# Optimization experiments

Measured on AMD Instinct MI355X. Metric: run time of the kernel, lower is better.

Reference implementation:

```python
import jax, jax.numpy as jnp
import numpy as np

N_NODES = 50000
N_EDGES = 800000


def gat_layer(h, src, dst, W, al, ar, b, n_dst):
    # h: [N, Fin]; W: [Fin, H*D]; al/ar: [H, D]; b: [H*D]
    H, D = al.shape
    z = (h @ W).reshape(-1, H, D)                      # [N, H, D]
    el = jnp.sum(z * al[None], axis=-1)                # [N, H]
    er = jnp.sum(z * ar[None], axis=-1)                # [N, H] (dst prefix == all nodes)
    e = jax.nn.leaky_relu(el[src] + er[dst], negative_slope=0.2)  # [E, H]
    emax = jax.ops.segment_max(e, dst, num_segments=n_dst)
    ee = jnp.exp(e - emax[dst])
    denom = jax.ops.segment_sum(ee, dst, num_segments=n_dst)
    alpha = ee / denom[dst]                            # [E, H]
    msg = alpha[:, :, None] * z[src]                   # [E, H, D]
    out = jax.ops.segment_sum(msg.reshape(-1, H * D), dst, num_segments=n_dst)
    return out + b                                     # [n_dst, H*D]


def setup_inputs() -> dict:
    key = jax.random.key(0)
    ks = jax.random.split(key, 16)
    hid, heads, dh = 256, 4, 64
    inp = {
        "x": jax.random.normal(ks[0], (N_NODES, 128), jnp.float32),
        "conv0_W": jax.random.normal(ks[1], (128, hid), jnp.float32) * 0.08,
        "conv0_al": jax.random.normal(ks[2], (heads, dh), jnp.float32) * 0.1,
        "conv0_ar": jax.random.normal(ks[3], (heads, dh), jnp.float32) * 0.1,
        "conv0_b": jnp.zeros((hid,), jnp.float32),
        "skip0_W": jax.random.normal(ks[4], (128, hid), jnp.float32) * 0.08,
        "skip0_b": jnp.zeros((hid,), jnp.float32),
        "conv1_W": jax.random.normal(ks[5], (hid, hid), jnp.float32) * 0.06,
        "conv1_al": jax.random.normal(ks[6], (heads, dh), jnp.float32) * 0.1,
        "conv1_ar": jax.random.normal(ks[7], (heads, dh), jnp.float32) * 0.1,
        "conv1_b": jnp.zeros((hid,), jnp.float32),
        "skip1_W": jax.random.normal(ks[8], (hid, hid), jnp.float32) * 0.06,
        "skip1_b": jnp.zeros((hid,), jnp.float32),
        "mlp_W1": jax.random.normal(ks[9], (hid, hid), jnp.float32) * 0.06,
        "mlp_b1": jnp.zeros((hid,), jnp.float32),
        "bn_gamma": jnp.ones((hid,), jnp.float32),
        "bn_beta": jnp.zeros((hid,), jnp.float32),
        "bn_mean": jnp.zeros((hid,), jnp.float32),
        "bn_var": jnp.ones((hid,), jnp.float32),
        "mlp_W2": jax.random.normal(ks[10], (hid, 47), jnp.float32) * 0.06,
        "mlp_b2": jnp.zeros((47,), jnp.float32),
        "edge_src": jax.random.randint(ks[11], (N_EDGES,), 0, N_NODES, jnp.int32),
        "edge_dst": jax.random.randint(ks[12], (N_EDGES,), 0, N_NODES, jnp.int32),
    }
    return inp


def reference(x, conv0_W, conv0_al, conv0_ar, conv0_b, skip0_W, skip0_b,
              conv1_W, conv1_al, conv1_ar, conv1_b, skip1_W, skip1_b,
              mlp_W1, mlp_b1, bn_gamma, bn_beta, bn_mean, bn_var,
              mlp_W2, mlp_b2, edge_src, edge_dst):
    n = x.shape[0]
    # layer 0: GAT conv + skip + ELU (dropout = identity in eval mode)
    h = gat_layer(x, edge_src, edge_dst, conv0_W, conv0_al, conv0_ar, conv0_b, n)
    h = jax.nn.elu(h + x @ skip0_W + skip0_b)
    # layer 1
    g = gat_layer(h, edge_src, edge_dst, conv1_W, conv1_al, conv1_ar, conv1_b, n)
    h = jax.nn.elu(g + h @ skip1_W + skip1_b)
    # MLP head: Linear -> BN(eval) -> ReLU -> (dropout id) -> Linear
    m = h @ mlp_W1 + mlp_b1
    m = (m - bn_mean) * (bn_gamma / jnp.sqrt(bn_var + 1e-5)) + bn_beta
    m = jax.nn.relu(m)
    logits = m @ mlp_W2 + mlp_b2
    return jax.nn.log_softmax(logits, axis=-1)
```

## Files before the change

### kernel.cpp

```cpp
#include <hip/hip_runtime.h>
#include <math.h>

#define NN 50000
#define NE 800000
#define HID 256
#define NH 4
#define DH 64
#define NB 196
#define CHUNK 4082

static inline int cdiv(int a, int b) { return (a + b - 1) / b; }

typedef __attribute__((ext_vector_type(8))) short short8;
typedef __attribute__((ext_vector_type(4))) short short4v;
typedef __attribute__((ext_vector_type(4))) float f32x4;
typedef __attribute__((ext_vector_type(2))) float f32x2;

__device__ inline unsigned short f2bf(float x) {
    union { float f; unsigned u; } v; v.f = x;
    unsigned r = v.u + 0x7FFFu + ((v.u >> 16) & 1u);
    return (unsigned short)(r >> 16);
}
__device__ inline float bf2f(unsigned short h) {
    union { unsigned u; float f; } v; v.u = ((unsigned)h) << 16;
    return v.f;
}
__device__ inline short8 zero8() {
    short8 z;
#pragma unroll
    for (int j = 0; j < 8; j++) z[j] = 0;
    return z;
}
__device__ inline unsigned char f2fp8(float x) {
    int p = __builtin_amdgcn_cvt_pk_fp8_f32(x, 0.f, 0, false);
    return (unsigned char)(p & 0xff);
}

__global__ __launch_bounds__(256) void p1_bucket_hist(const int* __restrict__ dst,
                                                      int* __restrict__ bcount) {
    __shared__ int h[NB];
    int tid = threadIdx.x;
    for (int i = tid; i < NB; i += 256) h[i] = 0;
    __syncthreads();
    int i0 = blockIdx.x * CHUNK;
    int n = min(CHUNK, NE - i0);
    for (int i = tid; i < n; i += 256) atomicAdd(&h[dst[i0 + i] >> 8], 1);
    __syncthreads();
    for (int i = tid; i < NB; i += 256)
        if (h[i]) atomicAdd(&bcount[i], h[i]);
}

__global__ __launch_bounds__(256) void p2_bucket_scan(const int* __restrict__ bcount,
                                                      int* __restrict__ bbase,
                                                      int* __restrict__ gcur) {
    __shared__ int s[256];
    int tid = threadIdx.x;
    int v = (tid < NB) ? bcount[tid] : 0;
    s[tid] = v;
    __syncthreads();
    for (int off = 1; off < 256; off <<= 1) {
        int t = (tid >= off) ? s[tid - off] : 0;
        __syncthreads();
        s[tid] += t;
        __syncthreads();
    }
    int ex = s[tid] - v;
    if (tid < NB) { bbase[tid] = ex; gcur[tid] = ex; }
    if (tid == NB - 1) bbase[NB] = s[tid];
}

__global__ __launch_bounds__(256) void p3_partition(
    const int* __restrict__ src, const int* __restrict__ dst,
    int* __restrict__ gcur, uint2* __restrict__ ebuf) {
    __shared__ int cnt[NB], loff[NB], cur[NB], gpos[NB];
    __shared__ int s[256];
    __shared__ uint2 buf[CHUNK];
    int tid = threadIdx.x;
    int i0 = blockIdx.x * CHUNK;
    int n = min(CHUNK, NE - i0);
    for (int i = tid; i < NB; i += 256) cnt[i] = 0;
    __syncthreads();
    for (int i = tid; i < n; i += 256) atomicAdd(&cnt[dst[i0 + i] >> 8], 1);
    __syncthreads();
    int v = (tid < NB) ? cnt[tid] : 0;
    s[tid] = v;
    __syncthreads();
    for (int off = 1; off < 256; off <<= 1) {
        int t = (tid >= off) ? s[tid - off] : 0;
        __syncthreads();
        s[tid] += t;
        __syncthreads();
    }
    if (tid < NB) {
        int ex = s[tid] - v;
        loff[tid] = ex;
        cur[tid] = ex;
        gpos[tid] = v ? atomicAdd(&gcur[tid], v) : 0;
    }
    __syncthreads();
    for (int i = tid; i < n; i += 256) {
        int d = dst[i0 + i];
        int sv = src[i0 + i];
        int p = atomicAdd(&cur[d >> 8], 1);
        buf[p] = make_uint2((unsigned)sv, (unsigned)d);
    }
    __syncthreads();
    for (int i = tid; i < n; i += 256) {
        uint2 e = buf[i];
        int b = (int)(e.y >> 8);
        ebuf[gpos[b] + (i - loff[b])] = e;
    }
}

__global__ __launch_bounds__(256) void p4_bucket_csr(
    const uint2* __restrict__ ebuf, const int* __restrict__ bbase,
    int* __restrict__ row_ptr, int* __restrict__ csr_src) {
    __shared__ int hist[256], cur[256], s[256];
    int b = blockIdx.x;
    int tid = threadIdx.x;
    int e0 = bbase[b], e1 = bbase[b + 1];
    hist[tid] = 0;
    __syncthreads();
    for (int i = e0 + tid; i < e1; i += 256)
        atomicAdd(&hist[ebuf[i].y & 255], 1);
    __syncthreads();
    int v = hist[tid];
    s[tid] = v;
    __syncthreads();
    for (int off = 1; off < 256; off <<= 1) {
        int t = (tid >= off) ? s[tid - off] : 0;
        __syncthreads();
        s[tid] += t;
        __syncthreads();
    }
    int pre = s[tid] - v;
    cur[tid] = pre;
    int d = b * 256 + tid;
    if (d < NN) row_ptr[d] = e0 + pre;
    if (b == NB - 1 && tid == 0) row_ptr[NN] = NE;
    __syncthreads();
    for (int i = e0 + tid; i < e1; i += 256) {
        uint2 e = ebuf[i];
        int p = atomicAdd(&cur[e.y & 255], 1);
        csr_src[e0 + p] = (int)e.x;
    }
}

__global__ void wcast_all_kernel(
    const float* __restrict__ c0W, const float* __restrict__ s0W,
    const float* __restrict__ c1W, const float* __restrict__ s1W,
    const float* __restrict__ m1W, const float* __restrict__ W2,
    const float* __restrict__ x,
    unsigned short* __restrict__ c0h, unsigned short* __restrict__ s0h,
    unsigned short* __restrict__ c1h, unsigned short* __restrict__ s1h,
    unsigned short* __restrict__ m1h, unsigned short* __restrict__ hWh,
    unsigned short* __restrict__ xh) {
    int i = blockIdx.x * blockDim.x + threadIdx.x;
    if (i >= 278528) {
        int j = i - 278528;
        if (j >= NN * 128 / 4) return;
        float4 v = ((const float4*)x)[j];
        short4v h;
        h[0] = (short)f2bf(v.x); h[1] = (short)f2bf(v.y);
        h[2] = (short)f2bf(v.z); h[3] = (short)f2bf(v.w);
        *(short4v*)&xh[j * 4] = h;
        return;
    }
    const float* W; unsigned short* H; int base; int head = 0;
    if (i < 32768)        { W = c0W; H = c0h; base = i; }
    else if (i < 65536)   { W = s0W; H = s0h; base = i - 32768; }
    else if (i < 131072)  { W = c1W; H = c1h; base = i - 65536; }
    else if (i < 196608)  { W = s1W; H = s1h; base = i - 131072; }
    else if (i < 262144)  { W = m1W; H = m1h; base = i - 196608; }
    else                  { W = W2;  H = hWh; base = i - 262144; head = 1; }
    float x_; int off;
    if (!head) {
        int k = base >> 8, n = base & 255;
        x_ = W[base];
        off = (k >> 5) * 8192 + (n >> 4) * 512 + ((k >> 3) & 3) * 128 + (n & 15) * 8 + (k & 7);
    } else {
        int k = base >> 6, n = base & 63;
        x_ = (n < 47) ? W[k * 47 + n] : 0.f;
        off = (k >> 5) * 2048 + (n >> 4) * 512 + ((k >> 3) & 3) * 128 + (n & 15) * 8 + (k & 7);
    }
    H[off] = f2bf(x_);
}

__global__ __launch_bounds__(256) void gemm_fused_kernel(
    const unsigned short* __restrict__ Ah,
    const unsigned short* __restrict__ Wc, const unsigned short* __restrict__ Ws,
    int M, int K,
    unsigned char* __restrict__ zb, unsigned short* __restrict__ sraw,
    const float* __restrict__ al, const float* __restrict__ ar,
    float* __restrict__ el, float* __restrict__ er) {
    __shared__ short sA[2][1024];

    int tid = threadIdx.x;
    int lane = tid & 63;
    int wid = tid >> 6;
    int m0 = blockIdx.x * 32;

    f32x4 accc[2][4], accs[2][4];
#pragma unroll
    for (int i = 0; i < 2; i++)
#pragma unroll
        for (int j = 0; j < 4; j++) {
            accc[i][j] = (f32x4){0.f, 0.f, 0.f, 0.f};
            accs[i][j] = (f32x4){0.f, 0.f, 0.f, 0.f};
        }

    bool stager = (tid < 128);
    int t7 = tid & 127;
    int r = t7 >> 2, kq = t7 & 3;
    int gr = m0 + r;
    size_t abase = (size_t)gr * K + kq * 8;
    int aoff = (r >> 4) * 512 + kq * 128 + (r & 15) * 8;

    int nkt = K >> 5;
    if (stager) {
        short8 sreg = zero8();
        if (gr < M) sreg = *(const short8*)(Ah + abase);
        *(short8*)(&sA[0][0] + aoff) = sreg;
    }
    __syncthreads();

    const unsigned short* bcp = Wc + (wid * 4) * 512 + lane * 8;
    const unsigned short* bsp = Ws + (wid * 4) * 512 + lane * 8;

    for (int kt = 0; kt < nkt; kt++) {
        short8 nreg = zero8();
        if (stager && kt + 1 < nkt && gr < M)
            nreg = *(const short8*)(Ah + abase + (size_t)(kt + 1) * 32);
        short8 bc[4], bs[4];
#pragma unroll
        for (int nf = 0; nf < 4; nf++) {
            bc[nf] = *(const short8*)(bcp + kt * 8192 + nf * 512);
            bs[nf] = *(const short8*)(bsp + kt * 8192 + nf * 512);
        }
        const short* cur = &sA[kt & 1][0];
        short8 ah[2];
#pragma unroll
        for (int mf = 0; mf < 2; mf++)
            ah[mf] = *(const short8*)(cur + mf * 512 + lane * 8);
#pragma unroll
        for (int nf = 0; nf < 4; nf++)
#pragma unroll
            for (int mf = 0; mf < 2; mf++) {
                accc[mf][nf] = __builtin_amdgcn_mfma_f32_16x16x32_bf16(ah[mf], bc[nf], accc[mf][nf], 0, 0, 0);
                accs[mf][nf] = __builtin_amdgcn_mfma_f32_16x16x32_bf16(ah[mf], bs[nf], accs[mf][nf], 0, 0, 0);
            }
        if (stager && kt + 1 < nkt)
            *(short8*)(&sA[(kt + 1) & 1][0] + aoff) = nreg;
        __syncthreads();
    }

#pragma unroll
    for (int mf = 0; mf < 2; mf++) {
        int row0 = m0 + mf * 16 + (lane >> 4) * 4;
#pragma unroll
        for (int reg = 0; reg < 4; reg++) {
            int row = row0 + reg;
            if (row >= M) continue;
            size_t rb = (size_t)row * HID;
#pragma unroll
            for (int nf = 0; nf < 4; nf++) {
                int col = wid * 64 + nf * 16 + (lane & 15);
                zb[rb + col] = f2fp8(accc[mf][nf][reg]);
                sraw[rb + col] = f2bf(accs[mf][nf][reg]);
            }
        }
    }

    {
        float alv[4], arv[4];
#pragma unroll
        for (int nf = 0; nf < 4; nf++) {
            int col = wid * 64 + nf * 16 + (lane & 15);
            alv[nf] = al[col];
            arv[nf] = ar[col];
        }
#pragma unroll
        for (int mf = 0; mf < 2; mf++) {
#pragma unroll
            for (int reg = 0; reg < 4; reg++) {
                float pl = 0.f, pr = 0.f;
#pragma unroll
                for (int nf = 0; nf < 4; nf++) {
                    pl = fmaf(accc[mf][nf][reg], alv[nf], pl);
                    pr = fmaf(accc[mf][nf][reg], arv[nf], pr);
                }
#pragma unroll
                for (int off = 8; off; off >>= 1) {
                    pl += __shfl_xor(pl, off);
                    pr += __shfl_xor(pr, off);
                }
                int row = m0 + mf * 16 + (lane >> 4) * 4 + reg;
                if ((lane & 15) == 0 && row < M) {
                    el[row * 4 + wid] = pl;
                    er[row * 4 + wid] = pr;
                }
            }
        }
    }
}

__global__ __launch_bounds__(256) void aggregate_kernel(
    const int* __restrict__ row_ptr, const int* __restrict__ csr_src,
    const float4* __restrict__ el4, const float4* __restrict__ er4,
    const unsigned char* __restrict__ zb, const float* __restrict__ conv_b,
    const unsigned short* __restrict__ sraw, const float* __restrict__ skip_b,
    unsigned short* __restrict__ outh, int n) {
    __shared__ float s_w[4][NH][64];
    __shared__ int s_s[4][64];
    int wid = threadIdx.x >> 6;
    int lane = threadIdx.x & 63;
    int node = blockIdx.x * 4 + wid;
    if (node >= n) return;
    int rb = row_ptr[node];
    int deg = row_ptr[node + 1] - rb;
    float4 ern = er4[node];
    float er_h[NH] = {ern.x, ern.y, ern.z, ern.w};
    int myh = lane >> 4;
    int f0 = lane * 4;

    float4 acc = make_float4(0.f, 0.f, 0.f, 0.f);
    float wsum[NH] = {0.f, 0.f, 0.f, 0.f};

    for (int c = 0; c < deg; c += 64) {
        int i = c + lane;
        int cnt = min(64, deg - c);
        if (i < deg) {
            int s = csr_src[rb + i];
            s_s[wid][lane] = s;
            float4 elv = el4[s];
            float ev[NH] = {elv.x, elv.y, elv.z, elv.w};
#pragma unroll
            for (int h = 0; h < NH; h++) {
                float e = ev[h] + er_h[h];
                e = (e > 0.f) ? e : 0.2f * e;
                float ee = __expf(e);
                s_w[wid][h][lane] = ee;
                wsum[h] += ee;
            }
        }
        __builtin_amdgcn_wave_barrier();
#pragma unroll 2
        for (int e = 0; e < cnt; e++) {
            int s = s_s[wid][e];
            unsigned zu = *(const unsigned*)(zb + (size_t)s * HID + f0);
            float wgt = s_w[wid][myh][e];
            f32x2 lo = __builtin_amdgcn_cvt_pk_f32_fp8((int)zu, false);
            f32x2 hi = __builtin_amdgcn_cvt_pk_f32_fp8((int)zu, true);
            acc.x = fmaf(wgt, lo[0], acc.x);
            acc.y = fmaf(wgt, lo[1], acc.y);
            acc.z = fmaf(wgt, hi[0], acc.z);
            acc.w = fmaf(wgt, hi[1], acc.w);
        }
        __builtin_amdgcn_wave_barrier();
    }
#pragma unroll
    for (int h = 0; h < NH; h++)
#pragma unroll
        for (int off = 32; off; off >>= 1) wsum[h] += __shfl_xor(wsum[h], off);
    float inv = (wsum[myh] > 0.f) ? 1.f / wsum[myh] : 0.f;
    float4 cb = *(const float4*)(conv_b + f0);
    float4 sb = *(const float4*)(skip_b + f0);
    uint2 sv = *(const uint2*)(sraw + (size_t)node * HID + f0);
    union { unsigned u; float f; } s0, s1, s2, s3;
    s0.u = sv.x << 16; s1.u = sv.x & 0xffff0000u;
    s2.u = sv.y << 16; s3.u = sv.y & 0xffff0000u;
    float v0 = acc.x * inv + cb.x + s0.f + sb.x;
    float v1 = acc.y * inv + cb.y + s1.f + sb.y;
    float v2 = acc.z * inv + cb.z + s2.f + sb.z;
    float v3 = acc.w * inv + cb.w + s3.f + sb.w;
    v0 = (v0 > 0.f) ? v0 : expm1f(v0);
    v1 = (v1 > 0.f) ? v1 : expm1f(v1);
    v2 = (v2 > 0.f) ? v2 : expm1f(v2);
    v3 = (v3 > 0.f) ? v3 : expm1f(v3);
    short4v o;
    o[0] = (short)f2bf(v0); o[1] = (short)f2bf(v1);
    o[2] = (short)f2bf(v2); o[3] = (short)f2bf(v3);
    *(short4v*)(outh + (size_t)node * HID + f0) = o;
}

__global__ __launch_bounds__(256) void gemm_bn_kernel(
    const unsigned short* __restrict__ Ah, const unsigned short* __restrict__ Bh_g,
    int M, int K, unsigned short* __restrict__ C,
    const float* __restrict__ bias, const float* __restrict__ g,
    const float* __restrict__ bt, const float* __restrict__ mean,
    const float* __restrict__ var) {
    __shared__ short sA[2][1024];
    int tid = threadIdx.x;
    int lane = tid & 63;
    int wid = tid >> 6;
    int m0 = blockIdx.x * 32;

    f32x4 acc[2][4];
#pragma unroll
    for (int i = 0; i < 2; i++)
#pragma unroll
        for (int j = 0; j < 4; j++) acc[i][j] = (f32x4){0.f, 0.f, 0.f, 0.f};

    bool stager = (tid < 128);
    int t7 = tid & 127;
    int r = t7 >> 2, kq = t7 & 3;
    int gr = m0 + r;
    size_t abase = (size_t)gr * K + kq * 8;
    int aoff = (r >> 4) * 512 + kq * 128 + (r & 15) * 8;

    int nkt = K >> 5;
    if (stager) {
        short8 sreg = zero8();
        if (gr < M) sreg = *(const short8*)(Ah + abase);
        *(short8*)(&sA[0][0] + aoff) = sreg;
    }
    __syncthreads();

    const unsigned short* bhp = Bh_g + (wid * 4) * 512 + lane * 8;

    for (int kt = 0; kt < nkt; kt++) {
        short8 nreg = zero8();
        if (stager && kt + 1 < nkt && gr < M)
            nreg = *(const short8*)(Ah + abase + (size_t)(kt + 1) * 32);
        short8 bh[4];
#pragma unroll
        for (int nf = 0; nf < 4; nf++)
            bh[nf] = *(const short8*)(bhp + kt * 8192 + nf * 512);
        const short* cur = &sA[kt & 1][0];
        short8 ah[2];
#pragma unroll
        for (int mf = 0; mf < 2; mf++)
            ah[mf] = *(const short8*)(cur + mf * 512 + lane * 8);
#pragma unroll
        for (int nf = 0; nf < 4; nf++)
#pragma unroll
            for (int mf = 0; mf < 2; mf++)
                acc[mf][nf] = __builtin_amdgcn_mfma_f32_16x16x32_bf16(ah[mf], bh[nf], acc[mf][nf], 0, 0, 0);
        if (stager && kt + 1 < nkt)
            *(short8*)(&sA[(kt + 1) & 1][0] + aoff) = nreg;
        __syncthreads();
    }

#pragma unroll
    for (int mf = 0; mf < 2; mf++) {
        int row0 = m0 + mf * 16 + (lane >> 4) * 4;
#pragma unroll
        for (int reg = 0; reg < 4; reg++) {
            int row = row0 + reg;
            if (row >= M) continue;
            size_t rb = (size_t)row * HID;
#pragma unroll
            for (int nf = 0; nf < 4; nf++) {
                int col = wid * 64 + nf * 16 + (lane & 15);
                float v = acc[mf][nf][reg];
                float s = g[col] * rsqrtf(var[col] + 1e-5f);
                v = (v + bias[col] - mean[col]) * s + bt[col];
                C[rb + col] = f2bf(fmaxf(v, 0.f));
            }
        }
    }
}

__global__ __launch_bounds__(256) void head_kernel(
    const unsigned short* __restrict__ Ah, const unsigned short* __restrict__ Bh_g,
    const float* __restrict__ b2, float* __restrict__ out, int M) {
    __shared__ short sA[2048];
    int tid = threadIdx.x;
    int lane = tid & 63;
    int wid = tid >> 6;
    int m0 = blockIdx.x * 64;

    f32x4 acc[4];
#pragma unroll
    for (int nf = 0; nf < 4; nf++) acc[nf] = (f32x4){0.f, 0.f, 0.f, 0.f};

    for (int kt = 0; kt < 8; kt++) {
        {
            int r = tid >> 2, kq = tid & 3;
            int gr = m0 + r;
            short8 h8 = zero8();
            if (gr < M) h8 = *(const short8*)(Ah + (size_t)gr * HID + kt * 32 + kq * 8);
            int off = (r >> 4) * 512 + kq * 128 + (r & 15) * 8;
            *(short8*)&sA[off] = h8;
        }
        __syncthreads();
        short8 ah = *(const short8*)&sA[wid * 512 + lane * 8];
#pragma unroll
        for (int nf = 0; nf < 4; nf++) {
            short8 bh = *(const short8*)(Bh_g + kt * 2048 + nf * 512 + lane * 8);
            acc[nf] = __builtin_amdgcn_mfma_f32_16x16x32_bf16(ah, bh, acc[nf], 0, 0, 0);
        }
        __syncthreads();
    }

    int col0 = lane & 15;
    float bias_[4];
#pragma unroll
    for (int nf = 0; nf < 4; nf++) {
        int col = nf * 16 + col0;
        bias_[nf] = (col < 47) ? b2[col] : 0.f;
    }
#pragma unroll
    for (int reg = 0; reg < 4; reg++) {
        int row = m0 + wid * 16 + (lane >> 4) * 4 + reg;
        float lg[4];
        float mx = -INFINITY;
#pragma unroll
        for (int nf = 0; nf < 4; nf++) {
            int col = nf * 16 + col0;
            float v = acc[nf][reg] + bias_[nf];
            lg[nf] = v;
            if (col < 47) mx = fmaxf(mx, v);
        }
#pragma unroll
        for (int off = 8; off; off >>= 1) mx = fmaxf(mx, __shfl_xor(mx, off));
        float s = 0.f;
#pragma unroll
        for (int nf = 0; nf < 4; nf++) {
            int col = nf * 16 + col0;
            if (col < 47) s += __expf(lg[nf] - mx);
        }
#pragma unroll
        for (int off = 8; off; off >>= 1) s += __shfl_xor(s, off);
        float li = logf(s);
        if (row < M) {
#pragma unroll
            for (int nf = 0; nf < 3; nf++) {
                int col = nf * 16 + col0;
                if (col < 47) out[(size_t)row * 47 + col] = lg[nf] - mx - li;
            }
        }
    }
}

extern "C" void kernel_launch(void* const* d_in, const int* in_sizes, int n_in,
                              void* d_out, int out_size, void* d_ws, size_t ws_size,
                              hipStream_t stream) {
    const float* x        = (const float*)d_in[0];
    const float* conv0_W  = (const float*)d_in[1];
    const float* conv0_al = (const float*)d_in[2];
    const float* conv0_ar = (const float*)d_in[3];
    const float* conv0_b  = (const float*)d_in[4];
    const float* skip0_W  = (const float*)d_in[5];
    const float* skip0_b  = (const float*)d_in[6];
    const float* conv1_W  = (const float*)d_in[7];
    const float* conv1_al = (const float*)d_in[8];
    const float* conv1_ar = (const float*)d_in[9];
    const float* conv1_b  = (const float*)d_in[10];
    const float* skip1_W  = (const float*)d_in[11];
    const float* skip1_b  = (const float*)d_in[12];
    const float* mlp_W1   = (const float*)d_in[13];
    const float* mlp_b1   = (const float*)d_in[14];
    const float* bn_gamma = (const float*)d_in[15];
    const float* bn_beta  = (const float*)d_in[16];
    const float* bn_mean  = (const float*)d_in[17];
    const float* bn_var   = (const float*)d_in[18];
    const float* mlp_W2   = (const float*)d_in[19];
    const float* mlp_b2   = (const float*)d_in[20];
    const int* edge_src   = (const int*)d_in[21];
    const int* edge_dst   = (const int*)d_in[22];
    float* out = (float*)d_out;

    char* w = (char*)d_ws;
    size_t off = 0;
    auto alloc = [&](size_t bytes) {
        char* p = w + off;
        off += (bytes + 255) & ~(size_t)255;
        return p;
    };
    int*    row_ptr = (int*)alloc((NN + 1) * sizeof(int));
    int*    bcount  = (int*)alloc(256 * sizeof(int));
    int*    bbase   = (int*)alloc(256 * sizeof(int));
    int*    gcur    = (int*)alloc(256 * sizeof(int));
    int*    csr_src = (int*)alloc(NE * sizeof(int));
    uint2*  ebuf    = (uint2*)alloc((size_t)NE * sizeof(uint2));
    float*  el      = (float*)alloc((size_t)NN * 4 * sizeof(float));
    float*  er      = (float*)alloc((size_t)NN * 4 * sizeof(float));
    unsigned char*  zb   = (unsigned char*)alloc((size_t)NN * HID * 2);
    unsigned short* sraw = (unsigned short*)alloc((size_t)NN * HID * 2);
    unsigned short* slA  = (unsigned short*)alloc((size_t)NN * HID * 2);
    unsigned short* hh   = (unsigned short*)alloc((size_t)NN * HID * 2);
    unsigned short* c0h = (unsigned short*)alloc(128 * 256 * 2);
    unsigned short* s0h = (unsigned short*)alloc(128 * 256 * 2);
    unsigned short* c1h = (unsigned short*)alloc(256 * 256 * 2);
    unsigned short* s1h = (unsigned short*)alloc(256 * 256 * 2);
    unsigned short* m1h = (unsigned short*)alloc(256 * 256 * 2);
    unsigned short* hWh = (unsigned short*)alloc(256 * 64 * 2);
    (void)ws_size;

    unsigned short* xh  = slA;
    unsigned short* h2h = slA;
    unsigned short* mh  = (unsigned short*)zb;

    int gemm_grid = cdiv(NN, 32);
    int head_grid = cdiv(NN, 64);
    int nodeblocks = cdiv(NN, 4);

    wcast_all_kernel<<<cdiv(278528 + NN * 128 / 4, 256), 256, 0, stream>>>(
        conv0_W, skip0_W, conv1_W, skip1_W, mlp_W1, mlp_W2, x,
        c0h, s0h, c1h, s1h, m1h, hWh, xh);

    hipMemsetAsync(bcount, 0, 256 * sizeof(int), stream);
    p1_bucket_hist<<<NB, 256, 0, stream>>>(edge_dst, bcount);
    p2_bucket_scan<<<1, 256, 0, stream>>>(bcount, bbase, gcur);
    p3_partition<<<NB, 256, 0, stream>>>(edge_src, edge_dst, gcur, ebuf);
    p4_bucket_csr<<<NB, 256, 0, stream>>>(ebuf, bbase, row_ptr, csr_src);

    gemm_fused_kernel<<<gemm_grid, 256, 0, stream>>>(xh, c0h, s0h, NN, 128,
        zb, sraw, conv0_al, conv0_ar, el, er);
    aggregate_kernel<<<nodeblocks, 256, 0, stream>>>(row_ptr, csr_src,
        (const float4*)el, (const float4*)er, zb, conv0_b, sraw, skip0_b, hh, NN);

    gemm_fused_kernel<<<gemm_grid, 256, 0, stream>>>(hh, c1h, s1h, NN, 256,
        zb, sraw, conv1_al, conv1_ar, el, er);
    aggregate_kernel<<<nodeblocks, 256, 0, stream>>>(row_ptr, csr_src,
        (const float4*)el, (const float4*)er, zb, conv1_b, sraw, skip1_b, h2h, NN);

    gemm_bn_kernel<<<gemm_grid, 256, 0, stream>>>(h2h, m1h, NN, 256,
        mh, mlp_b1, bn_gamma, bn_beta, bn_mean, bn_var);
    head_kernel<<<head_grid, 256, 0, stream>>>(mh, hWh, mlp_b2, out, NN);
}
```

Before: 246.4 us.

## Process four edges per wave in aggregation with 16-byte fp8 row loads

Restructures the GAT aggregation so each wave splits into four 16-lane groups, each handling a different neighbor edge, with every lane loading 16 fp8 features as a uint4 instead of 4 bytes. Edge scores are computed one head per lane group in 16-edge chunks, and partial accumulators are combined across groups with cross-lane shuffles at the end. The aim is more memory-level parallelism and wider gather loads for the feature rows. The cost is 16 accumulator registers per lane, a cross-group reduction, and select logic to pick outputs.

```diff
diff --git a/kernel.cpp b/kernel.cpp
--- a/kernel.cpp
+++ b/kernel.cpp
@@ -306,73 +306,102 @@
 
 __global__ __launch_bounds__(256) void aggregate_kernel(
     const int* __restrict__ row_ptr, const int* __restrict__ csr_src,
-    const float4* __restrict__ el4, const float4* __restrict__ er4,
+    const float* __restrict__ el, const float4* __restrict__ er4,
     const unsigned char* __restrict__ zb, const float* __restrict__ conv_b,
     const unsigned short* __restrict__ sraw, const float* __restrict__ skip_b,
     unsigned short* __restrict__ outh, int n) {
-    __shared__ float s_w[4][NH][64];
-    __shared__ int s_s[4][64];
+    __shared__ float s_w[4][NH][16];
+    __shared__ int s_s[4][16];
     int wid = threadIdx.x >> 6;
     int lane = threadIdx.x & 63;
     int node = blockIdx.x * 4 + wid;
     if (node >= n) return;
     int rb = row_ptr[node];
     int deg = row_ptr[node + 1] - rb;
+    int sl = lane & 15;
+    int grp = lane >> 4;
+    int myh = sl >> 2;
     float4 ern = er4[node];
-    float er_h[NH] = {ern.x, ern.y, ern.z, ern.w};
-    int myh = lane >> 4;
-    int f0 = lane * 4;
-
-    float4 acc = make_float4(0.f, 0.f, 0.f, 0.f);
-    float wsum[NH] = {0.f, 0.f, 0.f, 0.f};
-
-    for (int c = 0; c < deg; c += 64) {
-        int i = c + lane;
-        int cnt = min(64, deg - c);
+    float erh = (grp == 0) ? ern.x : (grp == 1) ? ern.y : (grp == 2) ? ern.z : ern.w;
+
+    float acc[16];
+#pragma unroll
+    for (int j = 0; j < 16; j++) acc[j] = 0.f;
+    float wloc = 0.f;
+
+    for (int c = 0; c < deg; c += 16) {
+        int i = c + sl;
+        int cnt = min(16, deg - c);
         if (i < deg) {
             int s = csr_src[rb + i];
-            s_s[wid][lane] = s;
-            float4 elv = el4[s];
-            float ev[NH] = {elv.x, elv.y, elv.z, elv.w};
-#pragma unroll
-            for (int h = 0; h < NH; h++) {
-                float e = ev[h] + er_h[h];
-                e = (e > 0.f) ? e : 0.2f * e;
-                float ee = __expf(e);
-                s_w[wid][h][lane] = ee;
-                wsum[h] += ee;
+            if (grp == 0) s_s[wid][sl] = s;
+            float e = el[(s << 2) + grp] + erh;
+            e = (e > 0.f) ? e : 0.2f * e;
+            float ee = __expf(e);
+            s_w[wid][grp][sl] = ee;
+            wloc += ee;
+        }
+        __builtin_amdgcn_wave_barrier();
+        for (int e4 = 0; e4 < cnt; e4 += 4) {
+            int ei = e4 + grp;
+            if (ei < cnt) {
+                int s = s_s[wid][ei];
+                float wgt = s_w[wid][myh][ei];
+                uint4 zv = *(const uint4*)(zb + (size_t)s * HID + sl * 16);
+                f32x2 d0 = __builtin_amdgcn_cvt_pk_f32_fp8((int)zv.x, false);
+                f32x2 d1 = __builtin_amdgcn_cvt_pk_f32_fp8((int)zv.x, true);
+                f32x2 d2 = __builtin_amdgcn_cvt_pk_f32_fp8((int)zv.y, false);
+                f32x2 d3 = __builtin_amdgcn_cvt_pk_f32_fp8((int)zv.y, true);
+                f32x2 d4 = __builtin_amdgcn_cvt_pk_f32_fp8((int)zv.z, false);
+                f32x2 d5 = __builtin_amdgcn_cvt_pk_f32_fp8((int)zv.z, true);
+                f32x2 d6 = __builtin_amdgcn_cvt_pk_f32_fp8((int)zv.w, false);
+                f32x2 d7 = __builtin_amdgcn_cvt_pk_f32_fp8((int)zv.w, true);
+                acc[0]  = fmaf(wgt, d0[0], acc[0]);
+                acc[1]  = fmaf(wgt, d0[1], acc[1]);
+                acc[2]  = fmaf(wgt, d1[0], acc[2]);
+                acc[3]  = fmaf(wgt, d1[1], acc[3]);
+                acc[4]  = fmaf(wgt, d2[0], acc[4]);
+                acc[5]  = fmaf(wgt, d2[1], acc[5]);
+                acc[6]  = fmaf(wgt, d3[0], acc[6]);
+                acc[7]  = fmaf(wgt, d3[1], acc[7]);
+                acc[8]  = fmaf(wgt, d4[0], acc[8]);
+                acc[9]  = fmaf(wgt, d4[1], acc[9]);
+                acc[10] = fmaf(wgt, d5[0], acc[10]);
+                acc[11] = fmaf(wgt, d5[1], acc[11]);
+                acc[12] = fmaf(wgt, d6[0], acc[12]);
+                acc[13] = fmaf(wgt, d6[1], acc[13]);
+                acc[14] = fmaf(wgt, d7[0], acc[14]);
+                acc[15] = fmaf(wgt, d7[1], acc[15]);
             }
         }
         __builtin_amdgcn_wave_barrier();
-#pragma unroll 2
-        for (int e = 0; e < cnt; e++) {
-            int s = s_s[wid][e];
-            unsigned zu = *(const unsigned*)(zb + (size_t)s * HID + f0);
-            float wgt = s_w[wid][myh][e];
-            f32x2 lo = __builtin_amdgcn_cvt_pk_f32_fp8((int)zu, false);
-            f32x2 hi = __builtin_amdgcn_cvt_pk_f32_fp8((int)zu, true);
-            acc.x = fmaf(wgt, lo[0], acc.x);
-            acc.y = fmaf(wgt, lo[1], acc.y);
-            acc.z = fmaf(wgt, hi[0], acc.z);
-            acc.w = fmaf(wgt, hi[1], acc.w);
-        }
-        __builtin_amdgcn_wave_barrier();
-    }
-#pragma unroll
-    for (int h = 0; h < NH; h++)
-#pragma unroll
-        for (int off = 32; off; off >>= 1) wsum[h] += __shfl_xor(wsum[h], off);
-    float inv = (wsum[myh] > 0.f) ? 1.f / wsum[myh] : 0.f;
-    float4 cb = *(const float4*)(conv_b + f0);
-    float4 sb = *(const float4*)(skip_b + f0);
-    uint2 sv = *(const uint2*)(sraw + (size_t)node * HID + f0);
+    }
+
+#pragma unroll
+    for (int off = 1; off < 16; off <<= 1) wloc += __shfl_xor(wloc, off);
+    float wsum_my = __shfl(wloc, myh << 4);
+    float inv = (wsum_my > 0.f) ? 1.f / wsum_my : 0.f;
+
+#pragma unroll
+    for (int j = 0; j < 16; j++) {
+        acc[j] += __shfl_xor(acc[j], 16);
+        acc[j] += __shfl_xor(acc[j], 32);
+    }
+
+#define SELA(k) ((grp & 2) ? ((grp & 1) ? acc[12 + (k)] : acc[8 + (k)]) \
+                           : ((grp & 1) ? acc[4 + (k)]  : acc[0 + (k)]))
+    int g0 = (sl << 4) + (grp << 2);
+    float4 cb = *(const float4*)(conv_b + g0);
+    float4 sb = *(const float4*)(skip_b + g0);
+    uint2 sv = *(const uint2*)(sraw + (size_t)node * HID + g0);
     union { unsigned u; float f; } s0, s1, s2, s3;
     s0.u = sv.x << 16; s1.u = sv.x & 0xffff0000u;
     s2.u = sv.y << 16; s3.u = sv.y & 0xffff0000u;
-    float v0 = acc.x * inv + cb.x + s0.f + sb.x;
-    float v1 = acc.y * inv + cb.y + s1.f + sb.y;
-    float v2 = acc.z * inv + cb.z + s2.f + sb.z;
-    float v3 = acc.w * inv + cb.w + s3.f + sb.w;
+    float v0 = SELA(0) * inv + cb.x + s0.f + sb.x;
+    float v1 = SELA(1) * inv + cb.y + s1.f + sb.y;
+    float v2 = SELA(2) * inv + cb.z + s2.f + sb.z;
+    float v3 = SELA(3) * inv + cb.w + s3.f + sb.w;
+#undef SELA
     v0 = (v0 > 0.f) ? v0 : expm1f(v0);
     v1 = (v1 > 0.f) ? v1 : expm1f(v1);
     v2 = (v2 > 0.f) ? v2 : expm1f(v2);
@@ -380,7 +409,7 @@
     short4v o;
     o[0] = (short)f2bf(v0); o[1] = (short)f2bf(v1);
     o[2] = (short)f2bf(v2); o[3] = (short)f2bf(v3);
-    *(short4v*)(outh + (size_t)node * HID + f0) = o;
+    *(short4v*)(outh + (size_t)node * HID + g0) = o;
 }
 
 __global__ __launch_bounds__(256) void gemm_bn_kernel(
@@ -609,12 +638,12 @@
     gemm_fused_kernel<<<gemm_grid, 256, 0, stream>>>(xh, c0h, s0h, NN, 128,
         zb, sraw, conv0_al, conv0_ar, el, er);
     aggregate_kernel<<<nodeblocks, 256, 0, stream>>>(row_ptr, csr_src,
-        (const float4*)el, (const float4*)er, zb, conv0_b, sraw, skip0_b, hh, NN);
+        el, (const float4*)er, zb, conv0_b, sraw, skip0_b, hh, NN);
 
     gemm_fused_kernel<<<gemm_grid, 256, 0, stream>>>(hh, c1h, s1h, NN, 256,
         zb, sraw, conv1_al, conv1_ar, el, er);
     aggregate_kernel<<<nodeblocks, 256, 0, stream>>>(row_ptr, csr_src,
-        (const float4*)el, (const float4*)er, zb, conv1_b, sraw, skip1_b, h2h, NN);
+        el, (const float4*)er, zb, conv1_b, sraw, skip1_b, h2h, NN);
 
     gemm_bn_kernel<<<gemm_grid, 256, 0, stream>>>(h2h, m1h, NN, 256,
         mh, mlp_b1, bn_gamma, bn_beta, bn_mean, bn_var);
```

New measurement: 245.6 us. Within noise of the previous version (-0.3%).
